# Optimization experiments

Hardware: AMD Instinct MI355X
Metric: run time of the kernel (lower is better)

## Reference

```python
import jax, jax.numpy as jnp
import numpy as np

B, N, K, M, CIN, O, OUT = 4, 1024, 30, 8, 9, 64, 512
BN_SCALE = 1.0 / np.sqrt(1.0 + 1e-5)  # eval-mode BatchNorm with default stats/affine


def setup_inputs() -> dict:
    key = jax.random.key(0)
    ks = jax.random.split(key, 8)
    x = jax.random.normal(ks[0], (B, CIN, N), jnp.float32)
    norm_plt = jax.random.normal(ks[1], (B, 3, N), jnp.float32)
    cls_label = jnp.zeros((B, 16), jnp.float32)
    conv1_w = jax.random.normal(ks[2], (64, 18), jnp.float32) * np.sqrt(2.0 / 18.0)
    conv1_b = jnp.zeros((64,), jnp.float32)
    sn_hw = jax.random.normal(ks[3], (4, 16, 28), jnp.float32) * np.sqrt(2.0 / 28.0)
    sn_ow = jax.random.normal(ks[4], (4, M, 16), jnp.float32) * np.sqrt(2.0 / 16.0)
    sn_ob = jnp.zeros((4, M), jnp.float32)
    mats = jax.random.normal(ks[5], (4, 2 * O, M * O), jnp.float32) * np.sqrt(2.0 / (2.0 * O))
    convt_w = jax.random.normal(ks[6], (OUT, 5 * O), jnp.float32) * np.sqrt(2.0 / (5.0 * O))
    return dict(x=x, norm_plt=norm_plt, cls_label=cls_label, conv1_w=conv1_w,
                conv1_b=conv1_b, sn_hw=sn_hw, sn_ow=sn_ow, sn_ob=sn_ob,
                mats=mats, convt_w=convt_w)


def _gather(feat, idx):
    # feat (B,N,C), idx (B,N,K) int -> (B,N,K,C): neighbor feature gather
    return jax.vmap(lambda f, i: f[i])(feat, idx)


def _bn(t):
    return t * BN_SCALE


def reference(x, norm_plt, cls_label, conv1_w, conv1_b, sn_hw, sn_ow, sn_ob, mats, convt_w):
    xt = jnp.transpose(x, (0, 2, 1))                       # (B,N,9)
    sq = jnp.sum(xt * xt, axis=-1)
    neg_d = 2.0 * jnp.einsum('bic,bjc->bij', xt, xt) - sq[:, :, None] - sq[:, None, :]
    _, idx = jax.lax.top_k(neg_d, K)                       # (B,N,K) knn indices

    nbr = _gather(xt, idx)                                 # (B,N,K,9)
    ctr = jnp.broadcast_to(xt[:, :, None, :], nbr.shape)   # (B,N,K,9)
    diff = nbr - ctr
    ed = jnp.linalg.norm(diff, axis=-1, keepdims=True)     # (B,N,K,1)
    xyz = jnp.concatenate([diff, nbr, ctr, ed], axis=-1)   # (B,N,K,28) scorenet input

    # get_graph_feature -> conv1 (1x1) -> BN -> relu -> max over k
    gf = jnp.concatenate([diff, ctr], axis=-1)             # (B,N,K,18)
    h = jax.nn.relu(_bn(jnp.einsum('bnkc,oc->bnko', gf, conv1_w) + conv1_b))
    x1 = jnp.max(h, axis=2)                                # (B,N,64)

    feats = [x1]
    f = x1
    for l in range(4):  # PAConv layers 2..5 (sequential, fixed count)
        hid = jax.nn.relu(_bn(jnp.einsum('bnkc,hc->bnkh', xyz, sn_hw[l])))
        score = jax.nn.softmax(jnp.einsum('bnkh,mh->bnkm', hid, sn_ow[l]) + sn_ob[l], axis=-1)
        kern = mats[l]                                     # (128, M*64)
        # feat_trans_dgcnn: neighbor uses full kernel on [f;f], center uses top half
        point = (jnp.concatenate([f, f], axis=-1) @ kern).reshape(B, N, M, O)
        center = (f @ kern[:O]).reshape(B, N, M, O)
        # assemble_dgcnn: sum_k sum_m score * (point[knn] - center)
        gp = _gather(point.reshape(B, N, M * O), idx).reshape(B, N, K, M, O)
        out = jnp.einsum('bnkm,bnkmo->bno', score, gp) - jnp.einsum('bnkm,bnmo->bno', score, center)
        f = jax.nn.relu(_bn(out))
        feats.append(f)

    xx = jnp.concatenate(feats, axis=-1)                   # (B,N,320)
    xc = jax.nn.relu(_bn(jnp.einsum('bnc,oc->bno', xx, convt_w)))
    return jnp.max(xc, axis=1)                             # (B,512) global max pool
```

## Files before the change

kernel.cpp:

```cpp
#include <hip/hip_runtime.h>
#include <hip/hip_bf16.h>

#define B 4
#define N 1024
#define KNN 30
#define MM 8
#define HID 16
#define FD 320
#define OUTC 512
#define BNS 0.9999950000374997f

typedef float f32x4 __attribute__((ext_vector_type(4)));
typedef short s16x8 __attribute__((ext_vector_type(8)));

#define OFF_IDX  0
#define OFF_CVT  122880
#define OFF_K2T  204800
#define OFF_FB   335872
#define OFF_SC   991232

#define L_HIST 0
#define L_JS   4096
#define L_BPN  4576
#define L_DIFF 4608
#define L_NBR  10368
#define L_CTR  16128
#define L_HWS  16272
#define L_OWS  23440
#define L_OBS  25488
#define K1_LDS 25616

__global__ void __launch_bounds__(256) k1(const float* __restrict__ x,
                                          const float* __restrict__ conv1_w,
                                          const float* __restrict__ conv1_b,
                                          const float* __restrict__ hw,
                                          const float* __restrict__ ow,
                                          const float* __restrict__ ob,
                                          const float* __restrict__ mats,
                                          const float* __restrict__ convt_w,
                                          int* __restrict__ idx,
                                          __hip_bfloat16* __restrict__ feats_bf,
                                          float* __restrict__ score,
                                          __hip_bfloat16* __restrict__ k2t_bf,
                                          __hip_bfloat16* __restrict__ cvt_bf,
                                          float* __restrict__ out) {
  __shared__ __align__(16) char pool[K1_LDS];
  int t = threadIdx.x;

  if (blockIdx.x >= 1024) {
    int pb = blockIdx.x - 1024;
    if (pb < 64) {
      float (*tile)[65] = (float(*)[65])pool;
      int l = pb >> 4, part = (pb >> 3) & 1, m = pb & 7;
      int tr = t >> 6, tc = t & 63;
      const float* src = mats + l * 65536 + (part * 64) * 512 + m * 64;
#pragma unroll
      for (int it = 0; it < 16; it++) { int c = it * 4 + tr; tile[c][tc] = src[c * 512 + tc]; }
      __syncthreads();
      __hip_bfloat16* dst = k2t_bf + l * 65536 + part * 512 + m * 64;
#pragma unroll
      for (int it = 0; it < 16; it++) { int o = it * 4 + tr; dst[o * 1024 + tc] = __float2bfloat16(tile[tc][o]); }
    } else {
      int id = (pb - 64) * 256 + t;
#pragma unroll
      for (int q = 0; q < 4; q++) {
        int i = id + q * 40960;
        cvt_bf[i] = __float2bfloat16(convt_w[i]);
      }
      if (id < B * OUTC) out[id] = 0.f;
    }
    return;
  }

  unsigned int* hist = (unsigned int*)(pool + L_HIST);
  int* js_l = (int*)(pool + L_JS);
  unsigned int* bp = (unsigned int*)(pool + L_BPN);
  int* bn = (int*)(pool + L_BPN + 16);
  float (*diff_s)[KNN][12] = (float(*)[KNN][12])(pool + L_DIFF);
  float (*nbr_s)[KNN][12] = (float(*)[KNN][12])(pool + L_NBR);
  float (*ctr_s)[9] = (float(*)[9])(pool + L_CTR);
  float* hws = (float*)(pool + L_HWS);
  float* ows = (float*)(pool + L_OWS);
  float* obs = (float*)(pool + L_OBS);

  int r = t >> 6, lane = t & 63;
  int row = blockIdx.x * 4 + r;
  int b = row >> 10;
  const float* xb = x + b * 9216;

  for (int i = t; i < 1792; i += 256) hws[i] = hw[i];
  for (int i = t; i < 512; i += 256) ows[i] = ow[i];
  if (t < 32) obs[t] = ob[t];
  if (t < 36) { int rr = t / 9, c = t - rr * 9; ctr_s[rr][c] = xb[c * 1024 + ((blockIdx.x * 4 + rr) & 1023)]; }

  int jrow = row & 1023;
  float cx[9];
#pragma unroll
  for (int c = 0; c < 9; c++) cx[c] = xb[c * 1024 + jrow];
  float sqn = 0.f;
#pragma unroll
  for (int c = 0; c < 9; c++) sqn = fmaf(cx[c], cx[c], sqn);
  unsigned int key[16];
#pragma unroll
  for (int s = 0; s < 16; s++) {
    int j = s * 64 + lane;
    float dot = 0.f, sbj = 0.f;
#pragma unroll
    for (int c = 0; c < 9; c++) {
      float xjc = xb[c * 1024 + j];
      dot = fmaf(cx[c], xjc, dot);
      sbj = fmaf(xjc, xjc, sbj);
    }
    float v = 2.0f * dot - sqn - sbj;
    unsigned u = __float_as_uint(v);
    key[s] = u ^ ((unsigned)(((int)u) >> 31) | 0x80000000u);
  }
  unsigned prefix = 0; int need = KNN;
  for (int p = 0; p < 4; p++) {
    int shift = 24 - 8 * p;
    for (int i = lane; i < 256; i += 64) hist[r * 256 + i] = 0;
    __syncthreads();
    unsigned himask = p ? (0xFFFFFFFFu << (shift + 8)) : 0u;
#pragma unroll
    for (int s = 0; s < 16; s++)
      if ((key[s] & himask) == prefix) atomicAdd(&hist[r * 256 + ((key[s] >> shift) & 255)], 1u);
    __syncthreads();
    int c0 = hist[r * 256 + 4 * lane], c1 = hist[r * 256 + 4 * lane + 1];
    int c2 = hist[r * 256 + 4 * lane + 2], c3 = hist[r * 256 + 4 * lane + 3];
    int lsum = c0 + c1 + c2 + c3, sfx = lsum;
#pragma unroll
    for (int ofs = 1; ofs < 64; ofs <<= 1) {
      int tt = __shfl_down(sfx, ofs, 64);
      if (lane + ofs < 64) sfx += tt;
    }
    int A3 = sfx - lsum, A2 = A3 + c3, A1 = A2 + c2, A0 = A1 + c1;
    if (A0 < need && need <= A0 + c0) { bp[r] = prefix | ((unsigned)(4 * lane + 0) << shift); bn[r] = need - A0; }
    if (A1 < need && need <= A1 + c1) { bp[r] = prefix | ((unsigned)(4 * lane + 1) << shift); bn[r] = need - A1; }
    if (A2 < need && need <= A2 + c2) { bp[r] = prefix | ((unsigned)(4 * lane + 2) << shift); bn[r] = need - A2; }
    if (A3 < need && need <= A3 + c3) { bp[r] = prefix | ((unsigned)(4 * lane + 3) << shift); bn[r] = need - A3; }
    __syncthreads();
    prefix = bp[r]; need = bn[r];
  }
  unsigned T = prefix;
  int* orow = idx + row * KNN;
  unsigned long long lowmask = (1ull << lane) - 1ull;
  int aboveBase = 0;
#pragma unroll
  for (int s = 0; s < 16; s++) {
    unsigned long long mA = __ballot(key[s] > T);
    if (key[s] > T) {
      int slot = aboveBase + __popcll(mA & lowmask);
      orow[slot] = s * 64 + lane;
      js_l[r * KNN + slot] = s * 64 + lane;
    }
    aboveBase += __popcll(mA);
  }
  int tieBase = 0;
  for (int s = 0; s < 16 && tieBase < need; s++) {
    unsigned long long mT = __ballot(key[s] == T);
    if (key[s] == T) {
      int rk = tieBase + __popcll(mT & lowmask);
      if (rk < need) {
        orow[aboveBase + rk] = s * 64 + lane;
        js_l[r * KNN + aboveBase + rk] = s * 64 + lane;
      }
    }
    tieBase += __popcll(mT);
  }
  __syncthreads();

  if (t < 120) {
    int rr = t / KNN, k = t - rr * KNN;
    int j = js_l[rr * KNN + k];
#pragma unroll
    for (int c = 0; c < 9; c++) {
      float nb = xb[c * 1024 + j];
      nbr_s[rr][k][c] = nb;
      diff_s[rr][k][c] = nb - ctr_s[rr][c];
    }
  }
  __syncthreads();

  {
    float wd[9];
#pragma unroll
    for (int c = 0; c < 9; c++) wd[c] = conv1_w[lane * 18 + c];
    float cd = 0.f;
#pragma unroll
    for (int c = 0; c < 9; c++) cd = fmaf(ctr_s[r][c], conv1_w[lane * 18 + 9 + c], cd);
    float best = -3.0e38f;
    for (int k = 0; k < KNN; k++) {
      const f32x4* dr = (const f32x4*)diff_s[r][k];
      f32x4 d0 = dr[0], d1 = dr[1], d2 = dr[2];
      float dd = 0.f;
      dd = fmaf(d0.x, wd[0], dd); dd = fmaf(d0.y, wd[1], dd);
      dd = fmaf(d0.z, wd[2], dd); dd = fmaf(d0.w, wd[3], dd);
      dd = fmaf(d1.x, wd[4], dd); dd = fmaf(d1.y, wd[5], dd);
      dd = fmaf(d1.z, wd[6], dd); dd = fmaf(d1.w, wd[7], dd);
      dd = fmaf(d2.x, wd[8], dd);
      best = fmaxf(best, dd);
    }
    float val = (best + cd + conv1_b[lane]) * BNS;
    feats_bf[row * FD + lane] = __float2bfloat16(fmaxf(val, 0.f));
  }

  for (int i = t; i < 480; i += 256) {
    int l = i / 120;
    int rem = i - l * 120;
    int rr = rem / KNN, k = rem - rr * KNN;
    float xv[28];
    float d2 = 0.f;
#pragma unroll
    for (int c = 0; c < 9; c++) {
      float df = diff_s[rr][k][c];
      xv[c] = df; xv[9 + c] = nbr_s[rr][k][c]; xv[18 + c] = ctr_s[rr][c];
      d2 = fmaf(df, df, d2);
    }
    xv[27] = sqrtf(d2);
    float hid[HID];
#pragma unroll
    for (int h = 0; h < HID; h++) {
      float a = 0.f;
#pragma unroll
      for (int c = 0; c < 28; c++) a = fmaf(xv[c], hws[l * 448 + h * 28 + c], a);
      hid[h] = fmaxf(a * BNS, 0.f);
    }
    float lg[MM], mx = -3.0e38f;
#pragma unroll
    for (int m = 0; m < MM; m++) {
      float a = obs[l * 8 + m];
#pragma unroll
      for (int h = 0; h < HID; h++) a = fmaf(hid[h], ows[l * 128 + m * 16 + h], a);
      lg[m] = a; mx = fmaxf(mx, a);
    }
    float s = 0.f;
#pragma unroll
    for (int m = 0; m < MM; m++) { lg[m] = __expf(lg[m] - mx); s += lg[m]; }
    float inv = 1.0f / s;
    int rowr = blockIdx.x * 4 + rr;
    float* so = score + l * 983040 + (rowr * KNN + k) * 8;
    *(float4*)so = make_float4(lg[0] * inv, lg[1] * inv, lg[2] * inv, lg[3] * inv);
    *(float4*)(so + 4) = make_float4(lg[4] * inv, lg[5] * inv, lg[6] * inv, lg[7] * inv);
  }
}

#define HSTR 1048
__global__ void __launch_bounds__(512) k_layer2(const int* __restrict__ idx,
                                                const float* __restrict__ score,
                                                const __hip_bfloat16* __restrict__ k2t_bf,
                                                __hip_bfloat16* __restrict__ feats_bf,
                                                const __hip_bfloat16* __restrict__ cvt_bf,
                                                float* __restrict__ out,
                                                int l, int last) {
  int row0 = blockIdx.x * 16;
  int t = threadIdx.x;
  int b = row0 >> 10;
  __shared__ int js[16][KNN];
  __shared__ float ssum[16][8];
  __shared__ __align__(16) __hip_bfloat16 Hs[16][HSTR];
  __shared__ __align__(16) __hip_bfloat16 ftile[16][336];
  __shared__ float pacc[8][16][16];
  const float* sc_l = score + l * 983040;
  for (int i = t; i < 16 * KNN; i += 512) {
    int r = i / KNN, k = i - r * KNN;
    js[r][k] = (b << 10) + idx[(row0 + r) * KNN + k];
  }
  if (t < 128) {
    int r = t >> 3, m = t & 7;
    float a = 0.f;
    for (int k = 0; k < KNN; k++) a += sc_l[(row0 + r) * 240 + k * 8 + m];
    ssum[r][m] = a;
  }
  __syncthreads();
  int w = t >> 6, lane = t & 63;
#pragma unroll
  for (int rr = 0; rr < 2; rr++) {
    int r = w * 2 + rr;
    int row = row0 + r;
    const float4* srow = (const float4*)(sc_l + row * 240);
    float g[MM] = {};
#pragma unroll 6
    for (int k = 0; k < KNN; k++) {
      float fv = __bfloat162float(feats_bf[js[r][k] * FD + l * 64 + lane]);
      float4 s0 = srow[2 * k], s1 = srow[2 * k + 1];
      g[0] = fmaf(s0.x, fv, g[0]); g[1] = fmaf(s0.y, fv, g[1]);
      g[2] = fmaf(s0.z, fv, g[2]); g[3] = fmaf(s0.w, fv, g[3]);
      g[4] = fmaf(s1.x, fv, g[4]); g[5] = fmaf(s1.y, fv, g[5]);
      g[6] = fmaf(s1.z, fv, g[6]); g[7] = fmaf(s1.w, fv, g[7]);
    }
    float fn = __bfloat162float(feats_bf[row * FD + l * 64 + lane]);
#pragma unroll
    for (int m = 0; m < MM; m++) {
      Hs[r][m * 64 + lane] = __float2bfloat16(g[m] - ssum[r][m] * fn);
      Hs[r][512 + m * 64 + lane] = __float2bfloat16(g[m]);
    }
  }
  __syncthreads();
  if (last) {
    const short* Fs = (const short*)feats_bf;
    {
      int r = t >> 5, c8 = (t & 31) * 8;
      *(s16x8*)&ftile[r][c8] = *(const s16x8*)(Fs + (row0 + r) * FD + c8);
    }
    __syncthreads();
  }
  int lr = lane & 15, lk8 = (lane >> 4) * 8;
  {
    int ct = w & 3, kh = w >> 2;
    const short* Ks2 = (const short*)(k2t_bf + l * 65536);
    const short* brow = Ks2 + (ct * 16 + lr) * 1024 + kh * 512 + lk8;
    const short* arow = (const short*)&Hs[lr][kh * 512 + lk8];
    f32x4 acc = {0.f, 0.f, 0.f, 0.f};
#pragma unroll 8
    for (int kk = 0; kk < 16; kk++) {
      s16x8 a = *(const s16x8*)(arow + kk * 32);
      s16x8 bb = *(const s16x8*)(brow + kk * 32);
      acc = __builtin_amdgcn_mfma_f32_16x16x32_bf16(a, bb, acc, 0, 0, 0);
    }
#pragma unroll
    for (int i = 0; i < 4; i++)
      pacc[w][(lane >> 4) * 4 + i][lr] = acc[i];
  }
  __syncthreads();
  if (w < 4) {
#pragma unroll
    for (int i = 0; i < 4; i++) {
      int ri = (lane >> 4) * 4 + i;
      float val = fmaxf((pacc[w][ri][lr] + pacc[w + 4][ri][lr]) * BNS, 0.f);
      __hip_bfloat16 vb = __float2bfloat16(val);
      if (!last) {
        feats_bf[(row0 + ri) * FD + (l + 1) * 64 + w * 16 + lr] = vb;
      } else {
        ftile[ri][256 + w * 16 + lr] = vb;
      }
    }
  }
  if (last) {
    __syncthreads();
    const short* Ws = (const short*)cvt_bf;
#pragma unroll
    for (int tn = 0; tn < 4; tn++) {
      int nb = w * 64 + tn * 16;
      const short* brow = Ws + (nb + lr) * FD + lk8;
      const short* arow = (const short*)&ftile[lr][lk8];
      f32x4 acc = {0.f, 0.f, 0.f, 0.f};
#pragma unroll
      for (int kk = 0; kk < 10; kk++) {
        s16x8 a = *(const s16x8*)(arow + kk * 32);
        s16x8 bb = *(const s16x8*)(brow + kk * 32);
        acc = __builtin_amdgcn_mfma_f32_16x16x32_bf16(a, bb, acc, 0, 0, 0);
      }
      float mx = fmaxf(fmaxf(acc[0], acc[1]), fmaxf(acc[2], acc[3]));
      mx = fmaxf(mx, __shfl_xor(mx, 16, 64));
      mx = fmaxf(mx, __shfl_xor(mx, 32, 64));
      if ((lane >> 4) == 0) {
        float val = fmaxf(mx * BNS, 0.f);
        atomicMax((unsigned int*)out + b * OUTC + nb + lr, __float_as_uint(val));
      }
    }
  }
}

extern "C" void kernel_launch(void* const* d_in, const int* in_sizes, int n_in,
                              void* d_out, int out_size, void* d_ws, size_t ws_size,
                              hipStream_t stream) {
  const float* x       = (const float*)d_in[0];
  const float* conv1_w = (const float*)d_in[3];
  const float* conv1_b = (const float*)d_in[4];
  const float* sn_hw   = (const float*)d_in[5];
  const float* sn_ow   = (const float*)d_in[6];
  const float* sn_ob   = (const float*)d_in[7];
  const float* mats    = (const float*)d_in[8];
  const float* convt_w = (const float*)d_in[9];
  float* out = (float*)d_out;

  float* wsp = (float*)d_ws;
  int* idx    = (int*)(wsp + OFF_IDX);
  __hip_bfloat16* cvt_bf = (__hip_bfloat16*)(wsp + OFF_CVT);
  __hip_bfloat16* k2t_bf = (__hip_bfloat16*)(wsp + OFF_K2T);
  __hip_bfloat16* feats_bf = (__hip_bfloat16*)(wsp + OFF_FB);
  float* score = wsp + OFF_SC;

  k1<<<1248, 256, 0, stream>>>(x, conv1_w, conv1_b, sn_hw, sn_ow, sn_ob,
                               mats, convt_w, idx, feats_bf, score,
                               k2t_bf, cvt_bf, out);
  for (int l = 0; l < 4; l++) {
    k_layer2<<<256, 512, 0, stream>>>(idx, score, k2t_bf, feats_bf,
                                      cvt_bf, out, l, l == 3 ? 1 : 0);
  }
}
```

Before: 189.2 us.

## Split kNN radix-select across two waves per row and precompute score sums

Result: faster. 183.0 us (-3.3%).

```diff
diff --git a/kernel.cpp b/kernel.cpp
--- a/kernel.cpp
+++ b/kernel.cpp
@@ -18,19 +18,20 @@
 #define OFF_K2T  204800
 #define OFF_FB   335872
 #define OFF_SC   991232
+#define OFF_SSUM 4923392
 
 #define L_HIST 0
-#define L_JS   4096
-#define L_BPN  4576
-#define L_DIFF 4608
-#define L_NBR  10368
-#define L_CTR  16128
-#define L_HWS  16272
-#define L_OWS  23440
-#define L_OBS  25488
-#define K1_LDS 25616
-
-__global__ void __launch_bounds__(256) k1(const float* __restrict__ x,
+#define L_JS   16384
+#define L_BPN  16864
+#define L_DIFF 16960
+#define L_NBR  22720
+#define L_CTR  28480
+#define L_HWS  28624
+#define L_OWS  35792
+#define L_OBS  37840
+#define K1_LDS 37968
+
+__global__ void __launch_bounds__(512) k1(const float* __restrict__ x,
                                           const float* __restrict__ conv1_w,
                                           const float* __restrict__ conv1_b,
                                           const float* __restrict__ hw,
@@ -41,6 +42,7 @@
                                           int* __restrict__ idx,
                                           __hip_bfloat16* __restrict__ feats_bf,
                                           float* __restrict__ score,
+                                          float* __restrict__ ssum_g,
                                           __hip_bfloat16* __restrict__ k2t_bf,
                                           __hip_bfloat16* __restrict__ cvt_bf,
                                           float* __restrict__ out) {
@@ -55,16 +57,16 @@
       int tr = t >> 6, tc = t & 63;
       const float* src = mats + l * 65536 + (part * 64) * 512 + m * 64;
 #pragma unroll
-      for (int it = 0; it < 16; it++) { int c = it * 4 + tr; tile[c][tc] = src[c * 512 + tc]; }
+      for (int it = 0; it < 8; it++) { int c = it * 8 + tr; tile[c][tc] = src[c * 512 + tc]; }
       __syncthreads();
       __hip_bfloat16* dst = k2t_bf + l * 65536 + part * 512 + m * 64;
 #pragma unroll
-      for (int it = 0; it < 16; it++) { int o = it * 4 + tr; dst[o * 1024 + tc] = __float2bfloat16(tile[tc][o]); }
+      for (int it = 0; it < 8; it++) { int o = it * 8 + tr; dst[o * 1024 + tc] = __float2bfloat16(tile[tc][o]); }
     } else {
-      int id = (pb - 64) * 256 + t;
-#pragma unroll
-      for (int q = 0; q < 4; q++) {
-        int i = id + q * 40960;
+      int id = (pb - 64) * 512 + t;
+#pragma unroll
+      for (int q = 0; q < 2; q++) {
+        int i = id + q * 81920;
         cvt_bf[i] = __float2bfloat16(convt_w[i]);
       }
       if (id < B * OUTC) out[id] = 0.f;
@@ -73,9 +75,12 @@
   }
 
   unsigned int* hist = (unsigned int*)(pool + L_HIST);
+  float (*pmax)[2][64] = (float(*)[2][64])(pool + L_HIST);
   int* js_l = (int*)(pool + L_JS);
   unsigned int* bp = (unsigned int*)(pool + L_BPN);
   int* bn = (int*)(pool + L_BPN + 16);
+  int* wAbv = (int*)(pool + L_BPN + 32);
+  int* wTie = (int*)(pool + L_BPN + 64);
   float (*diff_s)[KNN][12] = (float(*)[KNN][12])(pool + L_DIFF);
   float (*nbr_s)[KNN][12] = (float(*)[KNN][12])(pool + L_NBR);
   float (*ctr_s)[9] = (float(*)[9])(pool + L_CTR);
@@ -83,13 +88,14 @@
   float* ows = (float*)(pool + L_OWS);
   float* obs = (float*)(pool + L_OBS);
 
-  int r = t >> 6, lane = t & 63;
+  int w = t >> 6, lane = t & 63;
+  int r = w & 3, half = w >> 2;
   int row = blockIdx.x * 4 + r;
   int b = row >> 10;
   const float* xb = x + b * 9216;
 
-  for (int i = t; i < 1792; i += 256) hws[i] = hw[i];
-  for (int i = t; i < 512; i += 256) ows[i] = ow[i];
+  for (int i = t; i < 1792; i += 512) hws[i] = hw[i];
+  if (t < 512) ows[t] = ow[t];
   if (t < 32) obs[t] = ob[t];
   if (t < 36) { int rr = t / 9, c = t - rr * 9; ctr_s[rr][c] = xb[c * 1024 + ((blockIdx.x * 4 + rr) & 1023)]; }
 
@@ -100,10 +106,10 @@
   float sqn = 0.f;
 #pragma unroll
   for (int c = 0; c < 9; c++) sqn = fmaf(cx[c], cx[c], sqn);
-  unsigned int key[16];
-#pragma unroll
-  for (int s = 0; s < 16; s++) {
-    int j = s * 64 + lane;
+  unsigned int key[8];
+#pragma unroll
+  for (int s = 0; s < 8; s++) {
+    int j = (half * 8 + s) * 64 + lane;
     float dot = 0.f, sbj = 0.f;
 #pragma unroll
     for (int c = 0; c < 9; c++) {
@@ -116,56 +122,79 @@
     key[s] = u ^ ((unsigned)(((int)u) >> 31) | 0x80000000u);
   }
   unsigned prefix = 0; int need = KNN;
+  int sub = t & 3;
   for (int p = 0; p < 4; p++) {
     int shift = 24 - 8 * p;
-    for (int i = lane; i < 256; i += 64) hist[r * 256 + i] = 0;
+    for (int i = t; i < 4096; i += 512) hist[i] = 0;
     __syncthreads();
     unsigned himask = p ? (0xFFFFFFFFu << (shift + 8)) : 0u;
 #pragma unroll
-    for (int s = 0; s < 16; s++)
-      if ((key[s] & himask) == prefix) atomicAdd(&hist[r * 256 + ((key[s] >> shift) & 255)], 1u);
-    __syncthreads();
-    int c0 = hist[r * 256 + 4 * lane], c1 = hist[r * 256 + 4 * lane + 1];
-    int c2 = hist[r * 256 + 4 * lane + 2], c3 = hist[r * 256 + 4 * lane + 3];
-    int lsum = c0 + c1 + c2 + c3, sfx = lsum;
-#pragma unroll
-    for (int ofs = 1; ofs < 64; ofs <<= 1) {
-      int tt = __shfl_down(sfx, ofs, 64);
-      if (lane + ofs < 64) sfx += tt;
-    }
-    int A3 = sfx - lsum, A2 = A3 + c3, A1 = A2 + c2, A0 = A1 + c1;
-    if (A0 < need && need <= A0 + c0) { bp[r] = prefix | ((unsigned)(4 * lane + 0) << shift); bn[r] = need - A0; }
-    if (A1 < need && need <= A1 + c1) { bp[r] = prefix | ((unsigned)(4 * lane + 1) << shift); bn[r] = need - A1; }
-    if (A2 < need && need <= A2 + c2) { bp[r] = prefix | ((unsigned)(4 * lane + 2) << shift); bn[r] = need - A2; }
-    if (A3 < need && need <= A3 + c3) { bp[r] = prefix | ((unsigned)(4 * lane + 3) << shift); bn[r] = need - A3; }
+    for (int s = 0; s < 8; s++)
+      if ((key[s] & himask) == prefix)
+        atomicAdd(&hist[((r * 256 + ((key[s] >> shift) & 255)) << 2) | sub], 1u);
+    __syncthreads();
+    if (half == 0) {
+      int c0 = 0, c1 = 0, c2 = 0, c3 = 0;
+#pragma unroll
+      for (int q = 0; q < 4; q++) {
+        c0 += hist[((r * 256 + 4 * lane + 0) << 2) | q];
+        c1 += hist[((r * 256 + 4 * lane + 1) << 2) | q];
+        c2 += hist[((r * 256 + 4 * lane + 2) << 2) | q];
+        c3 += hist[((r * 256 + 4 * lane + 3) << 2) | q];
+      }
+      int lsum = c0 + c1 + c2 + c3, sfx = lsum;
+#pragma unroll
+      for (int ofs = 1; ofs < 64; ofs <<= 1) {
+        int tt = __shfl_down(sfx, ofs, 64);
+        if (lane + ofs < 64) sfx += tt;
+      }
+      int A3 = sfx - lsum, A2 = A3 + c3, A1 = A2 + c2, A0 = A1 + c1;
+      if (A0 < need && need <= A0 + c0) { bp[r] = prefix | ((unsigned)(4 * lane + 0) << shift); bn[r] = need - A0; }
+      if (A1 < need && need <= A1 + c1) { bp[r] = prefix | ((unsigned)(4 * lane + 1) << shift); bn[r] = need - A1; }
+      if (A2 < need && need <= A2 + c2) { bp[r] = prefix | ((unsigned)(4 * lane + 2) << shift); bn[r] = need - A2; }
+      if (A3 < need && need <= A3 + c3) { bp[r] = prefix | ((unsigned)(4 * lane + 3) << shift); bn[r] = need - A3; }
+    }
     __syncthreads();
     prefix = bp[r]; need = bn[r];
   }
   unsigned T = prefix;
+  {
+    int myA = 0, myT = 0;
+#pragma unroll
+    for (int s = 0; s < 8; s++) {
+      myA += __popcll(__ballot(key[s] > T));
+      myT += __popcll(__ballot(key[s] == T));
+    }
+    if (lane == 0) { wAbv[r * 2 + half] = myA; wTie[r * 2 + half] = myT; }
+  }
+  __syncthreads();
   int* orow = idx + row * KNN;
   unsigned long long lowmask = (1ull << lane) - 1ull;
-  int aboveBase = 0;
-#pragma unroll
-  for (int s = 0; s < 16; s++) {
-    unsigned long long mA = __ballot(key[s] > T);
-    if (key[s] > T) {
-      int slot = aboveBase + __popcll(mA & lowmask);
-      orow[slot] = s * 64 + lane;
-      js_l[r * KNN + slot] = s * 64 + lane;
-    }
-    aboveBase += __popcll(mA);
-  }
-  int tieBase = 0;
-  for (int s = 0; s < 16 && tieBase < need; s++) {
-    unsigned long long mT = __ballot(key[s] == T);
-    if (key[s] == T) {
-      int rk = tieBase + __popcll(mT & lowmask);
-      if (rk < need) {
-        orow[aboveBase + rk] = s * 64 + lane;
-        js_l[r * KNN + aboveBase + rk] = s * 64 + lane;
-      }
-    }
-    tieBase += __popcll(mT);
+  int aboveTotal = KNN - need;
+  {
+    int base = half ? wAbv[r * 2] : 0;
+#pragma unroll
+    for (int s = 0; s < 8; s++) {
+      unsigned long long mA = __ballot(key[s] > T);
+      if (key[s] > T) {
+        int slot = base + __popcll(mA & lowmask);
+        orow[slot] = (half * 8 + s) * 64 + lane;
+        js_l[r * KNN + slot] = (half * 8 + s) * 64 + lane;
+      }
+      base += __popcll(mA);
+    }
+    int tieBase = half ? wTie[r * 2] : 0;
+    for (int s = 0; s < 8 && tieBase < need; s++) {
+      unsigned long long mT = __ballot(key[s] == T);
+      if (key[s] == T) {
+        int rk = tieBase + __popcll(mT & lowmask);
+        if (rk < need) {
+          orow[aboveTotal + rk] = (half * 8 + s) * 64 + lane;
+          js_l[r * KNN + aboveTotal + rk] = (half * 8 + s) * 64 + lane;
+        }
+      }
+      tieBase += __popcll(mT);
+    }
   }
   __syncthreads();
 
@@ -185,11 +214,9 @@
     float wd[9];
 #pragma unroll
     for (int c = 0; c < 9; c++) wd[c] = conv1_w[lane * 18 + c];
-    float cd = 0.f;
-#pragma unroll
-    for (int c = 0; c < 9; c++) cd = fmaf(ctr_s[r][c], conv1_w[lane * 18 + 9 + c], cd);
     float best = -3.0e38f;
-    for (int k = 0; k < KNN; k++) {
+    int k0 = half * 15, k1e = k0 + 15;
+    for (int k = k0; k < k1e; k++) {
       const f32x4* dr = (const f32x4*)diff_s[r][k];
       f32x4 d0 = dr[0], d1 = dr[1], d2 = dr[2];
       float dd = 0.f;
@@ -200,13 +227,21 @@
       dd = fmaf(d2.x, wd[8], dd);
       best = fmaxf(best, dd);
     }
-    float val = (best + cd + conv1_b[lane]) * BNS;
-    feats_bf[row * FD + lane] = __float2bfloat16(fmaxf(val, 0.f));
-  }
-
-  for (int i = t; i < 480; i += 256) {
-    int l = i / 120;
-    int rem = i - l * 120;
+    pmax[r][half][lane] = best;
+    __syncthreads();
+    if (half == 0) {
+      float cd = 0.f;
+#pragma unroll
+      for (int c = 0; c < 9; c++) cd = fmaf(ctr_s[r][c], conv1_w[lane * 18 + 9 + c], cd);
+      float bestAll = fmaxf(pmax[r][0][lane], pmax[r][1][lane]);
+      float val = (bestAll + cd + conv1_b[lane]) * BNS;
+      feats_bf[row * FD + lane] = __float2bfloat16(fmaxf(val, 0.f));
+    }
+  }
+
+  if (t < 480) {
+    int l = t / 120;
+    int rem = t - l * 120;
     int rr = rem / KNN, k = rem - rr * KNN;
     float xv[28];
     float d2 = 0.f;
@@ -242,11 +277,22 @@
     *(float4*)so = make_float4(lg[0] * inv, lg[1] * inv, lg[2] * inv, lg[3] * inv);
     *(float4*)(so + 4) = make_float4(lg[4] * inv, lg[5] * inv, lg[6] * inv, lg[7] * inv);
   }
+  __syncthreads();
+
+  if (t < 128) {
+    int l = t >> 5, rr = (t >> 3) & 3, m = t & 7;
+    int rowr = blockIdx.x * 4 + rr;
+    const float* sl = score + l * 983040 + rowr * 240 + m;
+    float a = 0.f;
+    for (int k = 0; k < KNN; k++) a += sl[k * 8];
+    ssum_g[l * 32768 + rowr * 8 + m] = a;
+  }
 }
 
 #define HSTR 1048
 __global__ void __launch_bounds__(512) k_layer2(const int* __restrict__ idx,
                                                 const float* __restrict__ score,
+                                                const float* __restrict__ ssum_g,
                                                 const __hip_bfloat16* __restrict__ k2t_bf,
                                                 __hip_bfloat16* __restrict__ feats_bf,
                                                 const __hip_bfloat16* __restrict__ cvt_bf,
@@ -265,12 +311,7 @@
     int r = i / KNN, k = i - r * KNN;
     js[r][k] = (b << 10) + idx[(row0 + r) * KNN + k];
   }
-  if (t < 128) {
-    int r = t >> 3, m = t & 7;
-    float a = 0.f;
-    for (int k = 0; k < KNN; k++) a += sc_l[(row0 + r) * 240 + k * 8 + m];
-    ssum[r][m] = a;
-  }
+  if (t < 128) ssum[t >> 3][t & 7] = ssum_g[l * 32768 + (row0 + (t >> 3)) * 8 + (t & 7)];
   __syncthreads();
   int w = t >> 6, lane = t & 63;
 #pragma unroll
@@ -380,12 +421,13 @@
   __hip_bfloat16* k2t_bf = (__hip_bfloat16*)(wsp + OFF_K2T);
   __hip_bfloat16* feats_bf = (__hip_bfloat16*)(wsp + OFF_FB);
   float* score = wsp + OFF_SC;
-
-  k1<<<1248, 256, 0, stream>>>(x, conv1_w, conv1_b, sn_hw, sn_ow, sn_ob,
-                               mats, convt_w, idx, feats_bf, score,
+  float* ssum_g = wsp + OFF_SSUM;
+
+  k1<<<1248, 512, 0, stream>>>(x, conv1_w, conv1_b, sn_hw, sn_ow, sn_ob,
+                               mats, convt_w, idx, feats_bf, score, ssum_g,
                                k2t_bf, cvt_bf, out);
   for (int l = 0; l < 4; l++) {
-    k_layer2<<<256, 512, 0, stream>>>(idx, score, k2t_bf, feats_bf,
+    k_layer2<<<256, 512, 0, stream>>>(idx, score, ssum_g, k2t_bf, feats_bf,
                                       cvt_bf, out, l, l == 3 ? 1 : 0);
   }
 }
```
